# Kernel tuning notes

Measured on AMD Instinct MI355X. Metric: run time of the kernel, lower is better.

The kernel has to match this reference:

```python
import jax, jax.numpy as jnp
import numpy as np

EMB = 256
N_HEADS = 8
N_LVLS = 4
N_POINTS = 4
HEAD_DIM = EMB // N_HEADS  # 32
D_FFN = 1024
SHAPES = [(100, 100), (50, 50), (25, 25), (13, 13)]
LEN = sum(h * w for h, w in SHAPES)  # 13294
B = 4


def setup_inputs() -> dict:
    key = jax.random.key(0)
    ks = jax.random.split(key, 20)
    rn = lambda k, s, sc=0.02: jax.random.normal(k, s, jnp.float32) * sc
    starts = np.cumsum([0] + [h * w for h, w in SHAPES])[:-1]
    return {
        'features': jax.random.normal(ks[0], (B, LEN, EMB), jnp.float32),
        'pos': jax.random.normal(ks[1], (B, LEN, EMB), jnp.float32),
        'reference_points': jax.random.uniform(ks[2], (B, LEN, N_LVLS, 2), jnp.float32),
        'spatial_shapes': jnp.array(SHAPES, jnp.int32),
        'lvl_start_idx': jnp.array(starts, jnp.int32),
        'W_off': rn(ks[3], (EMB, N_HEADS * N_LVLS * N_POINTS * 2)),
        'b_off': rn(ks[4], (N_HEADS * N_LVLS * N_POINTS * 2,), 0.5),
        'W_attn': rn(ks[5], (EMB, N_HEADS * N_LVLS * N_POINTS)),
        'b_attn': rn(ks[6], (N_HEADS * N_LVLS * N_POINTS,)),
        'W_val': rn(ks[7], (EMB, EMB)),
        'b_val': rn(ks[8], (EMB,)),
        'W_out': rn(ks[9], (EMB, EMB)),
        'b_out': rn(ks[10], (EMB,)),
        'ln1_g': jnp.ones((EMB,), jnp.float32),
        'ln1_b': jnp.zeros((EMB,), jnp.float32),
        'W1': rn(ks[11], (EMB, D_FFN)),
        'b1': rn(ks[12], (D_FFN,)),
        'W2': rn(ks[13], (D_FFN, EMB)),
        'b2': rn(ks[14], (EMB,)),
        'ln2_g': jnp.ones((EMB,), jnp.float32),
        'ln2_b': jnp.zeros((EMB,), jnp.float32),
    }


def _layer_norm(x, g, b, eps=1e-5):
    mu = jnp.mean(x, axis=-1, keepdims=True)
    var = jnp.mean(jnp.square(x - mu), axis=-1, keepdims=True)
    return (x - mu) * jax.lax.rsqrt(var + eps) * g + b


def _ms_deform_attn(q, features, reference_points, shapes, starts,
                    W_off, b_off, W_attn, b_attn, W_val, b_val, W_out, b_out):
    Bn, Lq, D = features.shape
    value = (features @ W_val + b_val).reshape(Bn, Lq, N_HEADS, HEAD_DIM)
    off = (q @ W_off + b_off).reshape(Bn, Lq, N_HEADS, N_LVLS, N_POINTS, 2)
    attn = (q @ W_attn + b_attn).reshape(Bn, Lq, N_HEADS, N_LVLS * N_POINTS)
    attn = jax.nn.softmax(attn, axis=-1).reshape(Bn, Lq, N_HEADS, N_LVLS, N_POINTS)
    # normalizer per level is (W, H) for (x, y)
    norm = jnp.array([[w, h] for h, w in shapes], jnp.float32)  # (L, 2)
    loc = reference_points[:, :, None, :, None, :] + off / norm[None, None, None, :, None, :]

    out = jnp.zeros((Bn, N_HEADS, Lq, HEAD_DIM), value.dtype)
    for l, (H_, W_) in enumerate(shapes):
        s = starts[l]
        val = value[:, s:s + H_ * W_].transpose(0, 2, 1, 3)  # (B, nH, HW, Dh)
        locl = loc[:, :, :, l]  # (B, Lq, nH, P, 2), in [0,1]
        # grid_sample align_corners=False convention
        x = locl[..., 0] * W_ - 0.5
        y = locl[..., 1] * H_ - 0.5
        x0 = jnp.floor(x); y0 = jnp.floor(y)
        wx = x - x0; wy = y - y0
        x0i = x0.astype(jnp.int32); y0i = y0.astype(jnp.int32)

        def corner(xi, yi, w):
            valid = (xi >= 0) & (xi < W_) & (yi >= 0) & (yi < H_)
            idx = jnp.clip(yi, 0, H_ - 1) * W_ + jnp.clip(xi, 0, W_ - 1)  # (B, Lq, nH, P)
            idx = idx.transpose(0, 2, 1, 3).reshape(Bn, N_HEADS, Lq * N_POINTS, 1)
            g = jnp.take_along_axis(val, idx, axis=2)  # (B, nH, Lq*P, Dh)
            wm = (w * valid.astype(w.dtype)).transpose(0, 2, 1, 3).reshape(Bn, N_HEADS, Lq * N_POINTS, 1)
            return g * wm

        samp = (corner(x0i, y0i, (1 - wx) * (1 - wy))
                + corner(x0i + 1, y0i, wx * (1 - wy))
                + corner(x0i, y0i + 1, (1 - wx) * wy)
                + corner(x0i + 1, y0i + 1, wx * wy))
        samp = samp.reshape(Bn, N_HEADS, Lq, N_POINTS, HEAD_DIM)
        aw = attn[:, :, :, l].transpose(0, 2, 1, 3)  # (B, nH, Lq, P)
        out = out + jnp.einsum('bhqpd,bhqp->bhqd', samp, aw)

    out = out.transpose(0, 2, 1, 3).reshape(Bn, Lq, D)
    return out @ W_out + b_out


def reference(features, pos, reference_points, spatial_shapes, lvl_start_idx,
              W_off, b_off, W_attn, b_attn, W_val, b_val, W_out, b_out,
              ln1_g, ln1_b, W1, b1, W2, b2, ln2_g, ln2_b):
    shapes = [tuple(int(v) for v in r) for r in np.asarray(spatial_shapes)]
    starts = [int(v) for v in np.asarray(lvl_start_idx)]
    q = features + pos
    attn_out = _ms_deform_attn(q, features, reference_points, shapes, starts,
                               W_off, b_off, W_attn, b_attn, W_val, b_val, W_out, b_out)
    x = _layer_norm(features + attn_out, ln1_g, ln1_b)  # dropout is identity in eval
    ffn = jax.nn.relu(x @ W1 + b1) @ W2 + b2
    x = _layer_norm(x + ffn, ln2_g, ln2_b)  # stochastic depth is identity in eval
    return x
```

## Files before the change

### kernel.cpp

```cpp
#include <hip/hip_runtime.h>
#include <stdint.h>

#define LEN_T 13294
#define M_TOK 53176

typedef unsigned short u16;
typedef __bf16 bf16x8 __attribute__((ext_vector_type(8)));
typedef float f32x4 __attribute__((ext_vector_type(4)));
typedef float f32x2 __attribute__((ext_vector_type(2)));
typedef uint32_t u32x4 __attribute__((ext_vector_type(4)));
typedef uint32_t u32x2 __attribute__((ext_vector_type(2)));

__device__ __forceinline__ u16 f2bf(float f) {
    union { float f; uint32_t u; } v; v.f = f;
    uint32_t r = v.u + 0x7fffu + ((v.u >> 16) & 1u);
    return (u16)(r >> 16);
}
__device__ __forceinline__ float bf2f(u16 s) {
    union { uint32_t u; float f; } v; v.u = ((uint32_t)s) << 16;
    return v.f;
}
__device__ __forceinline__ u16 f2h(float f) {
    union { _Float16 h; u16 u; } c; c.h = (_Float16)f; return c.u;
}
__device__ __forceinline__ float hlo(uint32_t u) {
    union { uint32_t u; _Float16 h[2]; } v; v.u = u; return (float)v.h[0];
}
__device__ __forceinline__ float hhi(uint32_t u) {
    union { uint32_t u; _Float16 h[2]; } v; v.u = u; return (float)v.h[1];
}

__device__ __forceinline__ void gload_lds16(const u16* g, u16* l) {
    __builtin_amdgcn_global_load_lds(
        (const __attribute__((address_space(1))) uint32_t*)(g),
        (__attribute__((address_space(3))) uint32_t*)(l), 16, 0, 0);
}

__global__ __launch_bounds__(256) void prep_qf(
    const float* __restrict__ feat, const float* __restrict__ pos,
    u16* __restrict__ qb, u16* __restrict__ fb, int n4)
{
    int i = blockIdx.x * blockDim.x + threadIdx.x;
    int stride = gridDim.x * blockDim.x;
    for (; i < n4; i += stride) {
        float4 f = ((const float4*)feat)[i];
        float4 p = ((const float4*)pos)[i];
        uint32_t q0 = (uint32_t)f2bf(f.x + p.x) | ((uint32_t)f2bf(f.y + p.y) << 16);
        uint32_t q1 = (uint32_t)f2bf(f.z + p.z) | ((uint32_t)f2bf(f.w + p.w) << 16);
        uint32_t f0 = (uint32_t)f2bf(f.x) | ((uint32_t)f2bf(f.y) << 16);
        uint32_t f1 = (uint32_t)f2bf(f.z) | ((uint32_t)f2bf(f.w) << 16);
        ((uint2*)qb)[i] = make_uint2(q0, q1);
        ((uint2*)fb)[i] = make_uint2(f0, f1);
    }
}

__global__ __launch_bounds__(256) void wtrans_all(
    const float* __restrict__ W_val, const float* __restrict__ W_off,
    const float* __restrict__ W_attn, const float* __restrict__ W_out,
    const float* __restrict__ W1, const float* __restrict__ W2,
    u16* __restrict__ Wt_val, u16* __restrict__ Wt_oa,
    u16* __restrict__ Wt_out, u16* __restrict__ W1f, u16* __restrict__ W2f)
{
    int gid = blockIdx.x * 256 + threadIdx.x;
    if (gid < 229376) {
        const float* W; u16* D; int K, N, off;
        if      (gid < 65536)  { W = W_val;  D = Wt_val;        K = 256; N = 256; off = gid; }
        else if (gid < 131072) { W = W_off;  D = Wt_oa;         K = 256; N = 256; off = gid - 65536; }
        else if (gid < 163840) { W = W_attn; D = Wt_oa + 65536; K = 256; N = 128; off = gid - 131072; }
        else                   { W = W_out;  D = Wt_out;        K = 256; N = 256; off = gid - 163840; }
        int n = off / K, k = off - n * K;
        D[off] = f2bf(W[(size_t)k * N + n]);
    } else if (gid < 491520) {
        int off = gid - 229376;
        int e = off & 7, lane = (off >> 3) & 63;
        int r = off >> 9;
        int ks = r & 7, ni = (r >> 3) & 1, c = r >> 4;
        int col = c * 32 + ni * 16 + (lane & 15);
        int k = ks * 32 + (lane >> 4) * 8 + e;
        W1f[off] = f2bf(W1[(size_t)k * 1024 + col]);
    } else if (gid < 753664) {
        int off = gid - 491520;
        int e = off & 7, lane = (off >> 3) & 63;
        int r = off >> 9;
        int col = (r & 15) * 16 + (lane & 15);
        int k = (r >> 4) * 32 + (lane >> 4) * 8 + e;
        W2f[off] = f2bf(W2[(size_t)k * 256 + col]);
    }
}

#define MODE_VAL 0
#define MODE_OFFATTN 1

template<int MODE>
__global__ __launch_bounds__(256, 2) void gemm128(
    const u16* __restrict__ A, const u16* __restrict__ Bt,
    int M, int K,
    const float* __restrict__ bias, const float* __restrict__ bias2,
    void* __restrict__ out0, void* __restrict__ out1)
{
    __shared__ u16 Al[128 * 64];
    __shared__ u16 Bl[128 * 64];
    const int tid = threadIdx.x;
    const int lane = tid & 63;
    const int w = tid >> 6;
    const int wr = w >> 1, wc = w & 1;
    const int m0 = blockIdx.x * 128;
    const int n0 = blockIdx.y * 128;
    const int l15 = lane & 15;
    const int kg = lane >> 4;
    const int srow = lane >> 3;
    const int scol = (lane & 7) * 8;

    f32x4 acc[4][4];
#pragma unroll
    for (int i = 0; i < 4; ++i)
#pragma unroll
        for (int j = 0; j < 4; ++j)
            acc[i][j] = (f32x4){0.f, 0.f, 0.f, 0.f};

    const int nk = K >> 6;
    for (int kc = 0; kc < nk; ++kc) {
        __syncthreads();
#pragma unroll
        for (int j = 0; j < 4; ++j) {
            int c = w * 4 + j;
            int arow = m0 + c * 8 + srow;
            arow = arow < M ? arow : M - 1;
            gload_lds16(A + (size_t)arow * K + (kc << 6) + scol, Al + c * 512);
            int brow = n0 + c * 8 + srow;
            gload_lds16(Bt + (size_t)brow * K + (kc << 6) + scol, Bl + c * 512);
        }
        __syncthreads();
#pragma unroll
        for (int ks = 0; ks < 2; ++ks) {
            bf16x8 af[4], bfr[4];
#pragma unroll
            for (int i = 0; i < 4; ++i) {
                af[i]  = *(const bf16x8*)(Al + (wr * 64 + i * 16 + l15) * 64 + ks * 32 + kg * 8);
                bfr[i] = *(const bf16x8*)(Bl + (wc * 64 + i * 16 + l15) * 64 + ks * 32 + kg * 8);
            }
#pragma unroll
            for (int mi = 0; mi < 4; ++mi)
#pragma unroll
                for (int ni = 0; ni < 4; ++ni)
                    acc[mi][ni] = __builtin_amdgcn_mfma_f32_16x16x32_bf16(
                        af[mi], bfr[ni], acc[mi][ni], 0, 0, 0);
        }
    }

#pragma unroll
    for (int mi = 0; mi < 4; ++mi) {
#pragma unroll
        for (int r = 0; r < 4; ++r) {
            int row = m0 + wr * 64 + mi * 16 + kg * 4 + r;
            if (row >= M) continue;
#pragma unroll
            for (int ni = 0; ni < 4; ++ni) {
                int col = n0 + wc * 64 + ni * 16 + l15;
                float v = acc[mi][ni][r];
                if (MODE == MODE_VAL) {
                    int bI = row / LEN_T;
                    int t = row - bI * LEN_T;
                    int hh = col >> 5, d = col & 31;
                    ((u16*)out0)[((size_t)(bI * 8 + hh) * LEN_T + t) * 32 + d] =
                        f2h(v + bias[col]);
                } else {
                    if (col < 256) {
                        ((u16*)out0)[((size_t)(col >> 5) * M_TOK + row) * 32 + (col & 31)] =
                            f2h(v + bias[col]);
                    } else {
                        int c = col - 256;
                        ((u16*)out1)[((size_t)(c >> 4) * M_TOK + row) * 16 + (c & 15)] =
                            f2h(v + bias2[c]);
                    }
                }
            }
        }
    }
}

template<int KSTEPS, int OUTF32>
__global__ __launch_bounds__(256, 2) void gemm_ln(
    const u16* __restrict__ A, const u16* __restrict__ Bt,
    const float* __restrict__ bias, const u16* __restrict__ res,
    const float* __restrict__ g, const float* __restrict__ bb,
    u16* __restrict__ outb, float* __restrict__ outf, int M)
{
    __shared__ char ldsraw[66560];
    u16* Al = (u16*)ldsraw;
    u16* Bl = (u16*)(ldsraw + 8192);
    float* dump = (float*)ldsraw;
    const int tid = threadIdx.x;
    const int lane = tid & 63;
    const int w = tid >> 6;
    const int l15 = lane & 15;
    const int kg = lane >> 4;
    const int srow = lane >> 3;
    const int scol = (lane & 7) * 8;
    const int m0 = blockIdx.x * 64;
    const int K = KSTEPS * 64;

    f32x4 acc[4][4];
#pragma unroll
    for (int i = 0; i < 4; ++i)
#pragma unroll
        for (int j = 0; j < 4; ++j)
            acc[i][j] = (f32x4){0.f, 0.f, 0.f, 0.f};

    for (int kc = 0; kc < KSTEPS; ++kc) {
        __syncthreads();
#pragma unroll
        for (int j = 0; j < 2; ++j) {
            int c = w * 2 + j;
            int arow = m0 + c * 8 + srow;
            arow = arow < M ? arow : M - 1;
            gload_lds16(A + (size_t)arow * K + (kc << 6) + scol, Al + c * 512);
        }
#pragma unroll
        for (int j = 0; j < 8; ++j) {
            int c = w * 8 + j;
            int brow = c * 8 + srow;
            gload_lds16(Bt + (size_t)brow * K + (kc << 6) + scol, Bl + c * 512);
        }
        __syncthreads();
#pragma unroll
        for (int ks = 0; ks < 2; ++ks) {
            bf16x8 af[4], bfr[4];
#pragma unroll
            for (int i = 0; i < 4; ++i) {
                af[i]  = *(const bf16x8*)(Al + (i * 16 + l15) * 64 + ks * 32 + kg * 8);
                bfr[i] = *(const bf16x8*)(Bl + (w * 64 + i * 16 + l15) * 64 + ks * 32 + kg * 8);
            }
#pragma unroll
            for (int mi = 0; mi < 4; ++mi)
#pragma unroll
                for (int ni = 0; ni < 4; ++ni)
                    acc[mi][ni] = __builtin_amdgcn_mfma_f32_16x16x32_bf16(
                        af[mi], bfr[ni], acc[mi][ni], 0, 0, 0);
        }
    }

    __syncthreads();
#pragma unroll
    for (int mi = 0; mi < 4; ++mi) {
#pragma unroll
        for (int r = 0; r < 4; ++r) {
            int rr = mi * 16 + kg * 4 + r;
            int gr = m0 + rr; gr = gr < M ? gr : M - 1;
#pragma unroll
            for (int ni = 0; ni < 4; ++ni) {
                int col = w * 64 + ni * 16 + l15;
                dump[rr * 260 + col] = acc[mi][ni][r] + bias[col] +
                                       bf2f(res[(size_t)gr * 256 + col]);
            }
        }
    }
    __syncthreads();

    float4 gv = *(const float4*)(g + lane * 4);
    float4 bv = *(const float4*)(bb + lane * 4);
#pragma unroll
    for (int i = 0; i < 16; ++i) {
        int rr = w * 16 + i;
        float4 x = *(const float4*)(dump + rr * 260 + lane * 4);
        float s1 = x.x + x.y + x.z + x.w;
        float s2 = x.x*x.x + x.y*x.y + x.z*x.z + x.w*x.w;
#pragma unroll
        for (int o = 1; o < 64; o <<= 1) {
            s1 += __shfl_xor(s1, o);
            s2 += __shfl_xor(s2, o);
        }
        float mu = s1 * (1.0f / 256.0f);
        float var = s2 * (1.0f / 256.0f) - mu * mu;
        float rs = rsqrtf(var + 1e-5f);
        float o0 = (x.x - mu) * rs * gv.x + bv.x;
        float o1 = (x.y - mu) * rs * gv.y + bv.y;
        float o2 = (x.z - mu) * rs * gv.z + bv.z;
        float o3 = (x.w - mu) * rs * gv.w + bv.w;
        int grow = m0 + rr;
        if (grow < M) {
            if (OUTF32) {
                *(float4*)(outf + (size_t)grow * 256 + lane * 4) =
                    make_float4(o0, o1, o2, o3);
            } else {
                uint32_t u0 = (uint32_t)f2bf(o0) | ((uint32_t)f2bf(o1) << 16);
                uint32_t u1 = (uint32_t)f2bf(o2) | ((uint32_t)f2bf(o3) << 16);
                *(uint2*)(outb + (size_t)grow * 256 + lane * 4) = make_uint2(u0, u1);
            }
        }
    }
}

__global__ __launch_bounds__(256, 2) void ffn_fused(
    const u16* __restrict__ A, const u16* __restrict__ W1f, const u16* __restrict__ W2f,
    const float* __restrict__ b1, const float* __restrict__ b2,
    const float* __restrict__ g, const float* __restrict__ bb,
    float* __restrict__ outf, int M)
{
    __shared__ char lds[68608];
    u16* Axl = (u16*)lds;
    u16* ht0 = (u16*)(lds + 33792);
    u16* ht1 = (u16*)(lds + 33792 + 17408);
    float* dump = (float*)lds;
    const int tid = threadIdx.x;
    const int lane = tid & 63;
    const int w = tid >> 6;
    const int l15 = lane & 15;
    const int kg = lane >> 4;
    const int m0 = blockIdx.x * 64;

#pragma unroll
    for (int i = 0; i < 8; ++i) {
        int linear = i * 256 + tid;
        int row = linear >> 5;
        int gcol = (linear & 31) * 8;
        int grow = m0 + row; grow = grow < M ? grow : M - 1;
        uint4 v = *(const uint4*)(A + (size_t)grow * 256 + gcol);
        *(uint4*)(Axl + row * 264 + gcol) = v;
    }
    __syncthreads();

    f32x4 acc[4][4];
#pragma unroll
    for (int i = 0; i < 4; ++i)
#pragma unroll
        for (int j = 0; j < 4; ++j)
            acc[i][j] = (f32x4){0.f, 0.f, 0.f, 0.f};
    f32x4 acc2[4][2];

#define ZERO_ACC2() \
    _Pragma("unroll") for (int i = 0; i < 4; ++i) { \
        acc2[i][0] = (f32x4){0.f,0.f,0.f,0.f}; acc2[i][1] = (f32x4){0.f,0.f,0.f,0.f}; }

#define FFN1_CHUNK(HC) { \
    _Pragma("unroll") for (int ks = 0; ks < 8; ++ks) { \
        bf16x8 af[4], bw[2]; \
        _Pragma("unroll") for (int ni = 0; ni < 2; ++ni) \
            bw[ni] = *(const bf16x8*)(W1f + ((size_t)(((((HC) * 4 + w) * 2 + ni) * 8 + ks)) << 9) + lane * 8); \
        _Pragma("unroll") for (int mi = 0; mi < 4; ++mi) \
            af[mi] = *(const bf16x8*)(Axl + (mi * 16 + l15) * 264 + ks * 32 + kg * 8); \
        _Pragma("unroll") for (int mi = 0; mi < 4; ++mi) \
            _Pragma("unroll") for (int ni = 0; ni < 2; ++ni) \
                acc2[mi][ni] = __builtin_amdgcn_mfma_f32_16x16x32_bf16(af[mi], bw[ni], acc2[mi][ni], 0, 0, 0); \
    } }

#define FFN2_CHUNK(HC, HTR) { \
    _Pragma("unroll") for (int ks2 = 0; ks2 < 4; ++ks2) { \
        bf16x8 ah[4], bw2[4]; \
        _Pragma("unroll") for (int ni = 0; ni < 4; ++ni) \
            bw2[ni] = *(const bf16x8*)(W2f + ((size_t)((((HC) * 4 + ks2) * 16 + w * 4 + ni)) << 9) + lane * 8); \
        _Pragma("unroll") for (int mi = 0; mi < 4; ++mi) \
            ah[mi] = *(const bf16x8*)((HTR) + (mi * 16 + l15) * 136 + ks2 * 32 + kg * 8); \
        _Pragma("unroll") for (int mi = 0; mi < 4; ++mi) \
            _Pragma("unroll") for (int ni = 0; ni < 4; ++ni) \
                acc[mi][ni] = __builtin_amdgcn_mfma_f32_16x16x32_bf16(ah[mi], bw2[ni], acc[mi][ni], 0, 0, 0); \
    } }

#define HT_WRITE(HC, HTW) { \
    _Pragma("unroll") for (int mi = 0; mi < 4; ++mi) \
        _Pragma("unroll") for (int ni = 0; ni < 2; ++ni) \
            _Pragma("unroll") for (int r = 0; r < 4; ++r) { \
                int rr = mi * 16 + kg * 4 + r; \
                int cl = w * 32 + ni * 16 + l15; \
                float hv = acc2[mi][ni][r] + b1[(HC) * 128 + cl]; \
                (HTW)[rr * 136 + cl] = f2bf(hv > 0.f ? hv : 0.f); \
            } }

    ZERO_ACC2();
    FFN1_CHUNK(0);
    HT_WRITE(0, ht0);
    __syncthreads();

    for (int hc = 0; hc < 7; ++hc) {
        u16* htr = (hc & 1) ? ht1 : ht0;
        u16* htw = (hc & 1) ? ht0 : ht1;
        ZERO_ACC2();
        FFN1_CHUNK(hc + 1);
        FFN2_CHUNK(hc, htr);
        __syncthreads();
        HT_WRITE(hc + 1, htw);
        __syncthreads();
    }
    FFN2_CHUNK(7, ht1);

    __syncthreads();
#pragma unroll
    for (int mi = 0; mi < 4; ++mi) {
#pragma unroll
        for (int r = 0; r < 4; ++r) {
            int rr = mi * 16 + kg * 4 + r;
            int gr = m0 + rr; gr = gr < M ? gr : M - 1;
#pragma unroll
            for (int ni = 0; ni < 4; ++ni) {
                int col = w * 64 + ni * 16 + l15;
                dump[rr * 260 + col] = acc[mi][ni][r] + b2[col] +
                                       bf2f(A[(size_t)gr * 256 + col]);
            }
        }
    }
    __syncthreads();

    float4 gv = *(const float4*)(g + lane * 4);
    float4 bv = *(const float4*)(bb + lane * 4);
#pragma unroll
    for (int i = 0; i < 16; ++i) {
        int rr = w * 16 + i;
        float4 x = *(const float4*)(dump + rr * 260 + lane * 4);
        float s1 = x.x + x.y + x.z + x.w;
        float s2 = x.x*x.x + x.y*x.y + x.z*x.z + x.w*x.w;
#pragma unroll
        for (int o = 1; o < 64; o <<= 1) {
            s1 += __shfl_xor(s1, o);
            s2 += __shfl_xor(s2, o);
        }
        float mu = s1 * (1.0f / 256.0f);
        float var = s2 * (1.0f / 256.0f) - mu * mu;
        float rs = rsqrtf(var + 1e-5f);
        float o0 = (x.x - mu) * rs * gv.x + bv.x;
        float o1 = (x.y - mu) * rs * gv.y + bv.y;
        float o2 = (x.z - mu) * rs * gv.z + bv.z;
        float o3 = (x.w - mu) * rs * gv.w + bv.w;
        int grow = m0 + rr;
        if (grow < M) {
            *(float4*)(outf + (size_t)grow * 256 + lane * 4) =
                make_float4(o0, o1, o2, o3);
        }
    }
}

__device__ __forceinline__ void acc8h(u32x4 v, float w, float* acc) {
    acc[0] = fmaf(hlo(v.x), w, acc[0]);
    acc[1] = fmaf(hhi(v.x), w, acc[1]);
    acc[2] = fmaf(hlo(v.y), w, acc[2]);
    acc[3] = fmaf(hhi(v.y), w, acc[3]);
    acc[4] = fmaf(hlo(v.z), w, acc[4]);
    acc[5] = fmaf(hhi(v.z), w, acc[5]);
    acc[6] = fmaf(hlo(v.w), w, acc[6]);
    acc[7] = fmaf(hhi(v.w), w, acc[7]);
}

__global__ __launch_bounds__(256, 4) void sample_kernel(
    const u16* __restrict__ offt, const u16* __restrict__ attnt,
    const u16* __restrict__ value, const float* __restrict__ refp,
    u16* __restrict__ samp)
{
    int bid = blockIdx.x;
    int lb  = (bid & 7) * 832 + (bid >> 3);
    int bh  = lb / 208;
    int tblk = lb - bh * 208;
    int pr  = threadIdx.x >> 2;
    int dq  = threadIdx.x & 3;
    int tok = tblk * 64 + pr;
    if (tok >= LEN_T) return;
    int b = bh >> 3, h = bh & 7;
    int lane = threadIdx.x & 63;
    size_t row = (size_t)b * LEN_T + tok;

    int W_    = dq == 0 ? 100 : dq == 1 ? 50 : dq == 2 ? 25 : 13;
    float Wf   = dq == 0 ? 100.f : dq == 1 ? 50.f : dq == 2 ? 25.f : 13.f;
    float invW = dq == 0 ? 0.01f : dq == 1 ? 0.02f : dq == 2 ? 0.04f : (1.0f / 13.0f);

    u32x2 av = __builtin_nontemporal_load(
        (const u32x2*)(attnt + ((size_t)h * M_TOK + row) * 16 + dq * 4));
    float e0 = hlo(av.x), e1 = hhi(av.x), e2 = hlo(av.y), e3 = hhi(av.y);
    float m = fmaxf(fmaxf(e0, e1), fmaxf(e2, e3));
    m = fmaxf(m, __shfl_xor(m, 1));
    m = fmaxf(m, __shfl_xor(m, 2));
    e0 = __expf(e0 - m); e1 = __expf(e1 - m);
    e2 = __expf(e2 - m); e3 = __expf(e3 - m);
    float s = e0 + e1 + e2 + e3;
    s += __shfl_xor(s, 1);
    s += __shfl_xor(s, 2);
    float inv = 1.0f / s;
    float awp[4] = {e0 * inv, e1 * inv, e2 * inv, e3 * inv};

    f32x2 rv = __builtin_nontemporal_load((const f32x2*)(refp + row * 8 + dq * 2));
    float rx = rv.x, ry = rv.y;
    u32x4 ov = __builtin_nontemporal_load(
        (const u32x4*)(offt + ((size_t)h * M_TOK + row) * 32 + dq * 8));
    float dxs[4] = {hlo(ov.x), hlo(ov.y), hlo(ov.z), hlo(ov.w)};
    float dys[4] = {hhi(ov.x), hhi(ov.y), hhi(ov.z), hhi(ov.w)};

    float wts[16]; int offs[16];
#pragma unroll
    for (int p = 0; p < 4; ++p) {
        float x = fmaf(fmaf(dxs[p], invW, rx), Wf, -0.5f);
        float y = fmaf(fmaf(dys[p], invW, ry), Wf, -0.5f);
        float x0f = floorf(x), y0f = floorf(y);
        int x0 = (int)x0f, y0 = (int)y0f;
        int x1 = x0 + 1, y1 = y0 + 1;
        float wx = x - x0f, wy = y - y0f;
        float vx0 = ((unsigned)x0 < (unsigned)W_) ? 1.f : 0.f;
        float vx1 = ((unsigned)x1 < (unsigned)W_) ? 1.f : 0.f;
        float vy0 = ((unsigned)y0 < (unsigned)W_) ? 1.f : 0.f;
        float vy1 = ((unsigned)y1 < (unsigned)W_) ? 1.f : 0.f;
        int cx0 = min(max(x0, 0), W_ - 1);
        int cx1 = min(max(x1, 0), W_ - 1);
        int cy0 = min(max(y0, 0), W_ - 1);
        int cy1 = min(max(y1, 0), W_ - 1);
        float a = awp[p];
        wts[p*4+0] = (1.f - wx) * (1.f - wy) * a * vx0 * vy0;
        wts[p*4+1] = wx * (1.f - wy) * a * vx1 * vy0;
        wts[p*4+2] = (1.f - wx) * wy * a * vx0 * vy1;
        wts[p*4+3] = wx * wy * a * vx1 * vy1;
        offs[p*4+0] = (cy0 * W_ + cx0) * 32;
        offs[p*4+1] = (cy0 * W_ + cx1) * 32;
        offs[p*4+2] = (cy1 * W_ + cx0) * 32;
        offs[p*4+3] = (cy1 * W_ + cx1) * 32;
    }

    float acc[8];
#pragma unroll
    for (int d = 0; d < 8; ++d) acc[d] = 0.f;
    const int qbase = lane & ~3;

#pragma unroll
    for (int l2 = 0; l2 < 4; ++l2) {
        const int SL2 = (l2 == 0) ? 0 : (l2 == 1) ? 10000 : (l2 == 2) ? 12500 : 13125;
        const u16* vb = value + ((size_t)bh * LEN_T + SL2) * 32 + dq * 8;
        const int src = qbase + l2;
#pragma unroll
        for (int c2 = 0; c2 < 2; ++c2) {
            float w8[8]; int o8[8];
#pragma unroll
            for (int i = 0; i < 8; ++i) {
                w8[i] = __shfl(wts[c2*8 + i], src);
                o8[i] = __shfl(offs[c2*8 + i], src);
            }
            u32x4 vv[8];
#pragma unroll
            for (int i = 0; i < 8; ++i)
                vv[i] = *(const u32x4*)(vb + o8[i]);
#pragma unroll
            for (int i = 0; i < 8; ++i)
                acc8h(vv[i], w8[i], acc);
        }
    }
    u32x4 uo;
    uo.x = (uint32_t)f2bf(acc[0]) | ((uint32_t)f2bf(acc[1]) << 16);
    uo.y = (uint32_t)f2bf(acc[2]) | ((uint32_t)f2bf(acc[3]) << 16);
    uo.z = (uint32_t)f2bf(acc[4]) | ((uint32_t)f2bf(acc[5]) << 16);
    uo.w = (uint32_t)f2bf(acc[6]) | ((uint32_t)f2bf(acc[7]) << 16);
    __builtin_nontemporal_store(uo, (u32x4*)(samp + row * 256 + h * 32 + dq * 8));
}

extern "C" void kernel_launch(void* const* d_in, const int* in_sizes, int n_in,
                              void* d_out, int out_size, void* d_ws, size_t ws_size,
                              hipStream_t stream)
{
    const float* features = (const float*)d_in[0];
    const float* pos      = (const float*)d_in[1];
    const float* refp     = (const float*)d_in[2];
    const float* W_off  = (const float*)d_in[5];
    const float* b_off  = (const float*)d_in[6];
    const float* W_attn = (const float*)d_in[7];
    const float* b_attn = (const float*)d_in[8];
    const float* W_val  = (const float*)d_in[9];
    const float* b_val  = (const float*)d_in[10];
    const float* W_out  = (const float*)d_in[11];
    const float* b_out  = (const float*)d_in[12];
    const float* ln1_g  = (const float*)d_in[13];
    const float* ln1_b  = (const float*)d_in[14];
    const float* W1     = (const float*)d_in[15];
    const float* b1     = (const float*)d_in[16];
    const float* W2     = (const float*)d_in[17];
    const float* b2     = (const float*)d_in[18];
    const float* ln2_g  = (const float*)d_in[19];
    const float* ln2_b  = (const float*)d_in[20];
    float* out = (float*)d_out;

    char* ws = (char*)d_ws;
    size_t o = 0;
    auto alloc = [&](size_t bytes) { char* p = ws + o; o += (bytes + 255) & ~(size_t)255; return p; };
    u16* Wt_val = (u16*)alloc((size_t)256 * 256 * 2);
    u16* Wt_oa  = (u16*)alloc((size_t)384 * 256 * 2);
    u16* Wt_out = (u16*)alloc((size_t)256 * 256 * 2);
    u16* W1f    = (u16*)alloc((size_t)1024 * 256 * 2);
    u16* W2f    = (u16*)alloc((size_t)256 * 1024 * 2);
    u16* qb     = (u16*)alloc((size_t)M_TOK * 256 * 2);
    u16* fb     = (u16*)alloc((size_t)M_TOK * 256 * 2);
    char* big   = alloc((size_t)M_TOK * 1024 * 2);
    u16* value  = (u16*)big;
    u16* offt   = (u16*)(big + (size_t)M_TOK * 256 * 2);
    u16* attnt  = (u16*)(big + (size_t)M_TOK * 256 * 2 * 2);
    u16* samp = qb;
    u16* xb   = qb;

    dim3 blk(256);
    const int mb  = (M_TOK + 127) / 128;
    const int mb64 = (M_TOK + 63) / 64;

    prep_qf<<<2048, blk, 0, stream>>>(features, pos, qb, fb, M_TOK * 256 / 4);
    wtrans_all<<<2944, blk, 0, stream>>>(W_val, W_off, W_attn, W_out, W1, W2,
                                         Wt_val, Wt_oa, Wt_out, W1f, W2f);

    gemm128<MODE_VAL><<<dim3(mb, 2), blk, 0, stream>>>(
        fb, Wt_val, M_TOK, 256, b_val, nullptr, value, nullptr);
    gemm128<MODE_OFFATTN><<<dim3(mb, 3), blk, 0, stream>>>(
        qb, Wt_oa, M_TOK, 256, b_off, b_attn, offt, attnt);

    sample_kernel<<<6656, blk, 0, stream>>>(offt, attnt, value, refp, samp);

    gemm_ln<4, 0><<<mb64, blk, 0, stream>>>(
        samp, Wt_out, b_out, fb, ln1_g, ln1_b, xb, nullptr, M_TOK);

    ffn_fused<<<mb64, blk, 0, stream>>>(
        xb, W1f, W2f, b1, b2, ln2_g, ln2_b, out, M_TOK);
}
```

Baseline: 336.5 us.

## Shrink LDS footprint with bf16 LN staging and single hidden buffer for occupancy

Raises the launch bound from 2 to 3 blocks per CU for the GEMM, GEMM+LayerNorm and fused FFN kernels. To fit three blocks, the LayerNorm staging buffer is stored in bf16 instead of fp32, and the FFN's double-buffered hidden tile becomes a single buffer with reordered barriers. The FFN residual is now read from the A tile already in LDS instead of from global memory. The aim is more resident waves to hide memory latency. The cost is less overlap between FFN1 and FFN2, tighter register limits, and an extra bf16 rounding of the pre-LayerNorm sum.

```diff
diff --git a/kernel.cpp b/kernel.cpp
--- a/kernel.cpp
+++ b/kernel.cpp
@@ -92,7 +92,7 @@
 #define MODE_OFFATTN 1
 
 template<int MODE>
-__global__ __launch_bounds__(256, 2) void gemm128(
+__global__ __launch_bounds__(256, 3) void gemm128(
     const u16* __restrict__ A, const u16* __restrict__ Bt,
     int M, int K,
     const float* __restrict__ bias, const float* __restrict__ bias2,
@@ -180,16 +180,16 @@
 }
 
 template<int KSTEPS, int OUTF32>
-__global__ __launch_bounds__(256, 2) void gemm_ln(
+__global__ __launch_bounds__(256, 3) void gemm_ln(
     const u16* __restrict__ A, const u16* __restrict__ Bt,
     const float* __restrict__ bias, const u16* __restrict__ res,
     const float* __restrict__ g, const float* __restrict__ bb,
     u16* __restrict__ outb, float* __restrict__ outf, int M)
 {
-    __shared__ char ldsraw[66560];
+    __shared__ char ldsraw[40960];
     u16* Al = (u16*)ldsraw;
     u16* Bl = (u16*)(ldsraw + 8192);
-    float* dump = (float*)ldsraw;
+    u16* dumpb = (u16*)ldsraw;
     const int tid = threadIdx.x;
     const int lane = tid & 63;
     const int w = tid >> 6;
@@ -250,8 +250,8 @@
 #pragma unroll
             for (int ni = 0; ni < 4; ++ni) {
                 int col = w * 64 + ni * 16 + l15;
-                dump[rr * 260 + col] = acc[mi][ni][r] + bias[col] +
-                                       bf2f(res[(size_t)gr * 256 + col]);
+                dumpb[rr * 264 + col] = f2bf(acc[mi][ni][r] + bias[col] +
+                                             bf2f(res[(size_t)gr * 256 + col]));
             }
         }
     }
@@ -262,9 +262,11 @@
 #pragma unroll
     for (int i = 0; i < 16; ++i) {
         int rr = w * 16 + i;
-        float4 x = *(const float4*)(dump + rr * 260 + lane * 4);
-        float s1 = x.x + x.y + x.z + x.w;
-        float s2 = x.x*x.x + x.y*x.y + x.z*x.z + x.w*x.w;
+        uint2 raw = *(const uint2*)(dumpb + rr * 264 + lane * 4);
+        float x0 = bf2f((u16)(raw.x & 0xffff)), x1 = bf2f((u16)(raw.x >> 16));
+        float x2 = bf2f((u16)(raw.y & 0xffff)), x3 = bf2f((u16)(raw.y >> 16));
+        float s1 = x0 + x1 + x2 + x3;
+        float s2 = x0*x0 + x1*x1 + x2*x2 + x3*x3;
 #pragma unroll
         for (int o = 1; o < 64; o <<= 1) {
             s1 += __shfl_xor(s1, o);
@@ -273,10 +275,10 @@
         float mu = s1 * (1.0f / 256.0f);
         float var = s2 * (1.0f / 256.0f) - mu * mu;
         float rs = rsqrtf(var + 1e-5f);
-        float o0 = (x.x - mu) * rs * gv.x + bv.x;
-        float o1 = (x.y - mu) * rs * gv.y + bv.y;
-        float o2 = (x.z - mu) * rs * gv.z + bv.z;
-        float o3 = (x.w - mu) * rs * gv.w + bv.w;
+        float o0 = (x0 - mu) * rs * gv.x + bv.x;
+        float o1 = (x1 - mu) * rs * gv.y + bv.y;
+        float o2 = (x2 - mu) * rs * gv.z + bv.z;
+        float o3 = (x3 - mu) * rs * gv.w + bv.w;
         int grow = m0 + rr;
         if (grow < M) {
             if (OUTF32) {
@@ -291,17 +293,16 @@
     }
 }
 
-__global__ __launch_bounds__(256, 2) void ffn_fused(
+__global__ __launch_bounds__(256, 3) void ffn_fused(
     const u16* __restrict__ A, const u16* __restrict__ W1f, const u16* __restrict__ W2f,
     const float* __restrict__ b1, const float* __restrict__ b2,
     const float* __restrict__ g, const float* __restrict__ bb,
     float* __restrict__ outf, int M)
 {
-    __shared__ char lds[68608];
+    __shared__ char lds[51200];
     u16* Axl = (u16*)lds;
-    u16* ht0 = (u16*)(lds + 33792);
-    u16* ht1 = (u16*)(lds + 33792 + 17408);
-    float* dump = (float*)lds;
+    u16* ht  = (u16*)(lds + 33792);
+    u16* dumpb = (u16*)lds;
     const int tid = threadIdx.x;
     const int lane = tid & 63;
     const int w = tid >> 6;
@@ -344,57 +345,48 @@
                 acc2[mi][ni] = __builtin_amdgcn_mfma_f32_16x16x32_bf16(af[mi], bw[ni], acc2[mi][ni], 0, 0, 0); \
     } }
 
-#define FFN2_CHUNK(HC, HTR) { \
+#define FFN2_CHUNK(HC) { \
     _Pragma("unroll") for (int ks2 = 0; ks2 < 4; ++ks2) { \
         bf16x8 ah[4], bw2[4]; \
         _Pragma("unroll") for (int ni = 0; ni < 4; ++ni) \
             bw2[ni] = *(const bf16x8*)(W2f + ((size_t)((((HC) * 4 + ks2) * 16 + w * 4 + ni)) << 9) + lane * 8); \
         _Pragma("unroll") for (int mi = 0; mi < 4; ++mi) \
-            ah[mi] = *(const bf16x8*)((HTR) + (mi * 16 + l15) * 136 + ks2 * 32 + kg * 8); \
+            ah[mi] = *(const bf16x8*)(ht + (mi * 16 + l15) * 136 + ks2 * 32 + kg * 8); \
         _Pragma("unroll") for (int mi = 0; mi < 4; ++mi) \
             _Pragma("unroll") for (int ni = 0; ni < 4; ++ni) \
                 acc[mi][ni] = __builtin_amdgcn_mfma_f32_16x16x32_bf16(ah[mi], bw2[ni], acc[mi][ni], 0, 0, 0); \
     } }
 
-#define HT_WRITE(HC, HTW) { \
+#define HT_WRITE(HC) { \
     _Pragma("unroll") for (int mi = 0; mi < 4; ++mi) \
         _Pragma("unroll") for (int ni = 0; ni < 2; ++ni) \
             _Pragma("unroll") for (int r = 0; r < 4; ++r) { \
                 int rr = mi * 16 + kg * 4 + r; \
                 int cl = w * 32 + ni * 16 + l15; \
                 float hv = acc2[mi][ni][r] + b1[(HC) * 128 + cl]; \
-                (HTW)[rr * 136 + cl] = f2bf(hv > 0.f ? hv : 0.f); \
+                ht[rr * 136 + cl] = f2bf(hv > 0.f ? hv : 0.f); \
             } }
 
     ZERO_ACC2();
     FFN1_CHUNK(0);
-    HT_WRITE(0, ht0);
-    __syncthreads();
-
-    for (int hc = 0; hc < 7; ++hc) {
-        u16* htr = (hc & 1) ? ht1 : ht0;
-        u16* htw = (hc & 1) ? ht0 : ht1;
-        ZERO_ACC2();
-        FFN1_CHUNK(hc + 1);
-        FFN2_CHUNK(hc, htr);
+    for (int hc = 0; hc < 8; ++hc) {
         __syncthreads();
-        HT_WRITE(hc + 1, htw);
+        HT_WRITE(hc);
         __syncthreads();
-    }
-    FFN2_CHUNK(7, ht1);
-
-    __syncthreads();
+        FFN2_CHUNK(hc);
+        if (hc < 7) { ZERO_ACC2(); FFN1_CHUNK(hc + 1); }
+    }
+
 #pragma unroll
     for (int mi = 0; mi < 4; ++mi) {
 #pragma unroll
         for (int r = 0; r < 4; ++r) {
             int rr = mi * 16 + kg * 4 + r;
-            int gr = m0 + rr; gr = gr < M ? gr : M - 1;
 #pragma unroll
             for (int ni = 0; ni < 4; ++ni) {
                 int col = w * 64 + ni * 16 + l15;
-                dump[rr * 260 + col] = acc[mi][ni][r] + b2[col] +
-                                       bf2f(A[(size_t)gr * 256 + col]);
+                float v = acc[mi][ni][r] + b2[col] + bf2f(Axl[rr * 264 + col]);
+                dumpb[rr * 264 + col] = f2bf(v);
             }
         }
     }
@@ -405,9 +397,11 @@
 #pragma unroll
     for (int i = 0; i < 16; ++i) {
         int rr = w * 16 + i;
-        float4 x = *(const float4*)(dump + rr * 260 + lane * 4);
-        float s1 = x.x + x.y + x.z + x.w;
-        float s2 = x.x*x.x + x.y*x.y + x.z*x.z + x.w*x.w;
+        uint2 raw = *(const uint2*)(dumpb + rr * 264 + lane * 4);
+        float x0 = bf2f((u16)(raw.x & 0xffff)), x1 = bf2f((u16)(raw.x >> 16));
+        float x2 = bf2f((u16)(raw.y & 0xffff)), x3 = bf2f((u16)(raw.y >> 16));
+        float s1 = x0 + x1 + x2 + x3;
+        float s2 = x0*x0 + x1*x1 + x2*x2 + x3*x3;
 #pragma unroll
         for (int o = 1; o < 64; o <<= 1) {
             s1 += __shfl_xor(s1, o);
@@ -416,10 +410,10 @@
         float mu = s1 * (1.0f / 256.0f);
         float var = s2 * (1.0f / 256.0f) - mu * mu;
         float rs = rsqrtf(var + 1e-5f);
-        float o0 = (x.x - mu) * rs * gv.x + bv.x;
-        float o1 = (x.y - mu) * rs * gv.y + bv.y;
-        float o2 = (x.z - mu) * rs * gv.z + bv.z;
-        float o3 = (x.w - mu) * rs * gv.w + bv.w;
+        float o0 = (x0 - mu) * rs * gv.x + bv.x;
+        float o1 = (x1 - mu) * rs * gv.y + bv.y;
+        float o2 = (x2 - mu) * rs * gv.z + bv.z;
+        float o3 = (x3 - mu) * rs * gv.w + bv.w;
         int grow = m0 + rr;
         if (grow < M) {
             *(float4*)(outf + (size_t)grow * 256 + lane * 4) =
```

Result: no change. 336.2 us (-0.1%).
